# Kernel tuning notes

Measured on AMD Instinct MI355X. Metric: run time of the kernel, lower is better.

The kernel has to match this reference:

```python
import jax, jax.numpy as jnp
import numpy as np

SEQ_LEN = 4096
HIDDEN = 1280
NUM_HEADS = 16
HEAD_DIM = HIDDEN // NUM_HEADS  # 80
NUM_SEQS = 8


def setup_inputs() -> dict:
    key = jax.random.key(0)
    ks = jax.random.split(key, 8)
    x = jax.random.normal(ks[0], (SEQ_LEN, HIDDEN), dtype=jnp.float32)
    # rotary tables: use cos/sin of random angles so they are bounded like real RoPE tables
    ang = jax.random.uniform(ks[1], (SEQ_LEN, HEAD_DIM), dtype=jnp.float32) * 6.283185
    cos = jnp.cos(ang)
    sin = jnp.sin(ang)
    # variable-length packed segments: strictly increasing boundaries incl. 0 and SEQ_LEN
    rng = np.random.default_rng(0)
    inner = np.sort(rng.choice(np.arange(1, SEQ_LEN), size=NUM_SEQS - 1, replace=False))
    cu_seqlens = jnp.asarray(np.concatenate([[0], inner, [SEQ_LEN]]), dtype=jnp.int32)
    s = 0.02
    w_qkv = jax.random.normal(ks[2], (HIDDEN, 3 * HIDDEN), dtype=jnp.float32) * s
    b_qkv = jnp.zeros((3 * HIDDEN,), dtype=jnp.float32)
    w_proj = jax.random.normal(ks[3], (HIDDEN, HIDDEN), dtype=jnp.float32) * s
    b_proj = jnp.zeros((HIDDEN,), dtype=jnp.float32)
    return {"x": x, "cu_seqlens": cu_seqlens, "cos": cos, "sin": sin,
            "w_qkv": w_qkv, "b_qkv": b_qkv, "w_proj": w_proj, "b_proj": b_proj}


def _rotate_half(t):
    d = t.shape[-1] // 2
    return jnp.concatenate([-t[..., d:], t[..., :d]], axis=-1)


def _apply_rope(q, k, cos, sin):
    # q,k: (S,H,D); cos,sin: (S,D) broadcast over heads, computed in fp32
    c = cos[:, None, :].astype(jnp.float32)
    s = sin[:, None, :].astype(jnp.float32)
    qf, kf = q.astype(jnp.float32), k.astype(jnp.float32)
    q_out = qf * c + _rotate_half(qf) * s
    k_out = kf * c + _rotate_half(kf) * s
    return q_out.astype(q.dtype), k_out.astype(k.dtype)


def reference(x, cu_seqlens, cos, sin, w_qkv, b_qkv, w_proj, b_proj):
    S = x.shape[0]
    scale = HEAD_DIM ** (-0.5)
    qkv = (x @ w_qkv + b_qkv).reshape(S, 3, NUM_HEADS, HEAD_DIM)
    q, k, v = qkv[:, 0], qkv[:, 1], qkv[:, 2]  # each (S,H,D)
    q, k = _apply_rope(q, k, cos, sin)
    # block-diagonal varlen attention via segment-id mask (same math as per-chunk softmax)
    pos = jnp.arange(S)
    seg = jnp.searchsorted(cu_seqlens[1:], pos, side='right')  # (S,) segment id
    mask = seg[:, None] == seg[None, :]  # (S,S) block-diagonal
    scores = jnp.einsum('shd,thd->hst', q, k) * scale  # (H,S,S)
    scores = jnp.where(mask[None], scores.astype(jnp.float32), jnp.finfo(jnp.float32).min)
    attn = jax.nn.softmax(scores, axis=-1).astype(q.dtype)
    out = jnp.einsum('hst,thd->shd', attn, v).reshape(S, NUM_HEADS * HEAD_DIM)
    return out @ w_proj + b_proj
```

## Files before the change

kernel.cpp:

```cpp
#include <hip/hip_runtime.h>
#include <cstdint>
#include <cstddef>

typedef __bf16 bf16x8 __attribute__((ext_vector_type(8)));
typedef float f32x4 __attribute__((ext_vector_type(4)));
typedef float f32x16 __attribute__((ext_vector_type(16)));
typedef unsigned short u16x8 __attribute__((ext_vector_type(8)));

#define SEQ   4096
#define HID   1280
#define NH    16
#define HD    80

__device__ __forceinline__ unsigned short f2bf(float f) {
  unsigned int u = __float_as_uint(f);
  unsigned int r = u + 0x7FFFu + ((u >> 16) & 1u);
  return (unsigned short)(r >> 16);
}
__device__ __forceinline__ float bf2f(unsigned short h) {
  return __uint_as_float(((unsigned int)h) << 16);
}
__device__ __forceinline__ __bf16 us2bf(unsigned short u) {
  union { unsigned short s; __bf16 b; } c; c.s = u; return c.b;
}
__device__ __forceinline__ void dma16(const void* g, void* l) {
  __builtin_amdgcn_global_load_lds((const __attribute__((address_space(1))) unsigned int*)g,
                                   (__attribute__((address_space(3))) unsigned int*)l, 16, 0, 0);
}
__device__ __forceinline__ unsigned int cvtpk(float a, float b) {
  unsigned int w;
  asm("v_cvt_pk_bf16_f32 %0, %1, %2" : "=v"(w) : "v"(a), "v"(b));
  return w;
}
__device__ __forceinline__ float lo2f(unsigned int w) { return __uint_as_float(w << 16); }
__device__ __forceinline__ float hi2f(unsigned int w) { return __uint_as_float(w & 0xffff0000u); }

__global__ __launch_bounds__(256) void split_hi_kernel(const float* __restrict__ x,
                                                       unsigned short* __restrict__ hi,
                                                       int n4) {
  int i = blockIdx.x * 256 + threadIdx.x;
  if (i >= n4) return;
  float4 v = *((const float4*)x + i);
  *((ushort4*)hi + i) = make_ushort4(f2bf(v.x), f2bf(v.y), f2bf(v.z), f2bf(v.w));
}

__global__ __launch_bounds__(256) void tsplit_kernel(const float* __restrict__ W,
                                                     unsigned short* __restrict__ Thi,
                                                     unsigned short* __restrict__ Tlo,
                                                     int K, int N) {
  __shared__ float tile[32][33];
  int n0 = blockIdx.x * 32, k0 = blockIdx.y * 32;
  int tx = threadIdx.x & 31, ty = threadIdx.x >> 5;
#pragma unroll
  for (int i = 0; i < 32; i += 8)
    tile[ty + i][tx] = W[(size_t)(k0 + ty + i) * N + n0 + tx];
  __syncthreads();
#pragma unroll
  for (int i = 0; i < 32; i += 8) {
    float v = tile[tx][ty + i];
    size_t idx = (size_t)(n0 + ty + i) * K + (size_t)(k0 + tx);
    unsigned short h = f2bf(v);
    Thi[idx] = h;
    Tlo[idx] = f2bf(v - bf2f(h));
  }
}

__global__ __launch_bounds__(256, 3) void gemm128_x2(
    const unsigned short* __restrict__ A, const unsigned short* __restrict__ Bh,
    const unsigned short* __restrict__ Bl, const float* __restrict__ bias,
    float* __restrict__ out0, float* __restrict__ out1, float* __restrict__ out2,
    int M, int N, int K) {
  __shared__ __align__(16) unsigned short sALL[3 * 8192];

  const int t = threadIdx.x;
  const int lane = t & 63, wave = t >> 6;
  const int c16 = lane & 15, quad = lane >> 4;
  const int bm = blockIdx.y * 128, bn = blockIdx.x * 128;
  const int wr = (wave >> 1) * 64, wc = (wave & 1) * 64;
  const int lrow = lane >> 3;
  const int lswz = (lane & 7) ^ lrow;

  f32x4 acc[4][4];
#pragma unroll
  for (int i = 0; i < 4; ++i)
#pragma unroll
    for (int j = 0; j < 4; ++j) acc[i][j] = (f32x4){0.f, 0.f, 0.f, 0.f};

  const unsigned short* gp[12];
#pragma unroll
  for (int i = 0; i < 12; ++i) {
    const int ua = wave * 12 + i;
    const int arr = ua >> 4, sub = ua & 15;
    const unsigned short* g = (arr == 0) ? A : (arr == 1) ? Bh : Bl;
    const int rowg = ((arr == 0) ? bm : bn) + sub * 8 + lrow;
    gp[i] = g + (size_t)rowg * K + lswz * 8;
  }

  for (int k0 = 0; k0 < K; k0 += 64) {
    __syncthreads();
#pragma unroll
    for (int i = 0; i < 12; ++i)
      dma16(gp[i] + k0, &sALL[(wave * 12 + i) * 512]);
    __syncthreads();
#pragma unroll
    for (int ks = 0; ks < 2; ++ks) {
      bf16x8 a[4], bh[4], bl[4];
#pragma unroll
      for (int mi = 0; mi < 4; ++mi) {
        const int row = wr + mi * 16 + c16;
        const int off = row * 64 + (((ks * 4 + quad) ^ (row & 7)) * 8);
        a[mi] = *(const bf16x8*)&sALL[off];
      }
#pragma unroll
      for (int ni = 0; ni < 4; ++ni) {
        const int row = wc + ni * 16 + c16;
        const int off = row * 64 + (((ks * 4 + quad) ^ (row & 7)) * 8);
        bh[ni] = *(const bf16x8*)&sALL[8192 + off];
        bl[ni] = *(const bf16x8*)&sALL[16384 + off];
      }
#pragma unroll
      for (int mi = 0; mi < 4; ++mi)
#pragma unroll
        for (int ni = 0; ni < 4; ++ni) {
          acc[mi][ni] = __builtin_amdgcn_mfma_f32_16x16x32_bf16(a[mi], bh[ni], acc[mi][ni], 0, 0, 0);
          acc[mi][ni] = __builtin_amdgcn_mfma_f32_16x16x32_bf16(a[mi], bl[ni], acc[mi][ni], 0, 0, 0);
        }
    }
  }
#pragma unroll
  for (int ni = 0; ni < 4; ++ni) {
    int colg = bn + wc + ni * 16 + c16;
    float bv = bias[colg];
    float* op;
    int c = colg;
    if (c < 1280) op = out0;
    else if (c < 2560) { op = out1; c -= 1280; }
    else { op = out2; c -= 2560; }
#pragma unroll
    for (int mi = 0; mi < 4; ++mi)
#pragma unroll
      for (int r = 0; r < 4; ++r) {
        int rowg = bm + wr + mi * 16 + quad * 4 + r;
        op[(size_t)rowg * 1280 + c] = acc[mi][ni][r] + bv;
      }
  }
}

__global__ __launch_bounds__(256) void rope_pack_kernel(
    float* __restrict__ qf, const float* __restrict__ kf,
    const float* __restrict__ cs, const float* __restrict__ sn,
    unsigned short* __restrict__ khi, unsigned short* __restrict__ klo) {
  const int h = blockIdx.y;
  const int s = blockIdx.x * 64 + (threadIdx.x >> 2);
  const int p = threadIdx.x & 3;
  float* qrow = qf + (size_t)s * HID + h * HD;
  const float* krow = kf + (size_t)s * HID + h * HD;
  const float* cr = cs + (size_t)s * HD;
  const float* sr = sn + (size_t)s * HD;
  unsigned short* kh = khi + ((size_t)h * SEQ + s) * HD;
  unsigned short* kl = klo + ((size_t)h * SEQ + s) * HD;
#pragma unroll
  for (int j = 0; j < 10; ++j) {
    int d = 10 * p + j;
    float c0 = cr[d], s0 = sr[d], c1 = cr[d + 40], s1 = sr[d + 40];
    float q0 = qrow[d], q1 = qrow[d + 40];
    qrow[d]      = q0 * c0 - q1 * s0;
    qrow[d + 40] = q1 * c1 + q0 * s1;
    float k0 = krow[d], k1 = krow[d + 40];
    float kn0 = k0 * c0 - k1 * s0;
    float kn1 = k1 * c1 + k0 * s1;
    unsigned short h0 = f2bf(kn0), h1 = f2bf(kn1);
    kh[d] = h0;      kl[d] = f2bf(kn0 - bf2f(h0));
    kh[d + 40] = h1; kl[d + 40] = f2bf(kn1 - bf2f(h1));
  }
}

__global__ __launch_bounds__(256) void vt_pack_kernel(const float* __restrict__ vf,
                                                      unsigned short* __restrict__ vthi,
                                                      unsigned short* __restrict__ vtlo) {
  __shared__ unsigned short sTh[80][72];
  __shared__ unsigned short sTl[80][72];
  const int h = blockIdx.y;
  const int s0 = blockIdx.x * 64;
  const int t = threadIdx.x;
  {
    int row = t >> 2, p = (t & 3) * 20;
    const float* src = vf + (size_t)(s0 + row) * HID + h * HD + p;
#pragma unroll
    for (int i = 0; i < 5; ++i) {
      float4 v = *(const float4*)(src + 4 * i);
      float vv[4] = {v.x, v.y, v.z, v.w};
#pragma unroll
      for (int j = 0; j < 4; ++j) {
        int d = p + 4 * i + j;
        unsigned short hu = f2bf(vv[j]);
        sTh[d][row] = hu;
        sTl[d][row] = f2bf(vv[j] - bf2f(hu));
      }
    }
  }
  __syncthreads();
  if (t < 160) {
    int d = t >> 1, half = (t & 1) * 32;
    size_t base = (size_t)(h * HD + d) * SEQ + s0 + half;
#pragma unroll
    for (int i = 0; i < 8; ++i) {
      *(ushort4*)&vthi[base + 4 * i] = *(ushort4*)&sTh[d][half + 4 * i];
      *(ushort4*)&vtlo[base + 4 * i] = *(ushort4*)&sTl[d][half + 4 * i];
    }
  }
}


#define MFMA32(A, B, C) __builtin_amdgcn_mfma_f32_32x32x16_bf16(A, B, C, 0, 0, 0)

__global__ __launch_bounds__(128, 2) void attn_kernel(
    const float* __restrict__ qf, const unsigned short* __restrict__ khi,
    const unsigned short* __restrict__ klo, const unsigned short* __restrict__ vthi,
    const unsigned short* __restrict__ vtlo, const int* __restrict__ cu,
    unsigned short* __restrict__ ohi) {
  __shared__ __align__(16) unsigned short sAll[20480];
  unsigned short* const sKh = sAll;
  unsigned short* const sKl = sAll + 5120;
  unsigned short* const sVh = sAll + 10240;
  unsigned short* const sVl = sAll + 15360;

  const int t = threadIdx.x;
  const int lane = t & 63, wave = t >> 6;
  const int ln5 = lane & 31;
  const int hi  = lane >> 5;
  const int ln7 = lane & 7;
  const int lr8 = lane >> 3;
  const int vswz = (lane & 7) ^ lr8;

  const unsigned int u = (blockIdx.x & 7) * 128 + (blockIdx.x >> 3);
  const int h = (int)(u >> 6);
  const int r0 = (int)(u & 63u) * 64;

  int cu_r[9];
#pragma unroll
  for (int i = 0; i < 9; ++i) cu_r[i] = cu[i];

  const int q_my = r0 + wave * 32 + ln5;
  int sq = 0, sg0 = 0, sg1 = 0;
#pragma unroll
  for (int i = 1; i < 8; ++i) {
    sq  += (q_my    >= cu_r[i]) ? 1 : 0;
    sg0 += (r0      >= cu_r[i]) ? 1 : 0;
    sg1 += (r0 + 63 >= cu_r[i]) ? 1 : 0;
  }
  const int kb_lo = cu_r[sq], kb_hi = cu_r[sq + 1];
  const int ck0 = cu_r[sg0] & ~63;
  const int kend = cu_r[sg1 + 1];
  const int nchunk = (kend - ck0 + 63) >> 6;

  int ccol[5];
#pragma unroll
  for (int c = 0; c < 5; ++c)
    ccol[c] = (c < 4) ? ((((2 * c) + hi) ^ ln7) * 8) : ((8 + hi) * 8);

  int koff[10];
#pragma unroll
  for (int i = 0; i < 10; ++i) {
    const int G = i * 64 + lane;
    const int key = (G * 205) >> 11;
    const int p = G - key * 10;
    const int cl = (p < 8) ? (p ^ (key & 7)) : p;
    koff[i] = key * 80 + cl * 8;
  }

  const float qsc = 0.11180339887498949f;
  bf16x8 qh[5], ql[5];
  {
    const float* qrow = qf + (size_t)q_my * HID + h * HD;
#pragma unroll
    for (int kt = 0; kt < 5; ++kt) {
      const int d0 = kt * 16 + hi * 8;
      float4 a0 = *(const float4*)(qrow + d0);
      float4 a1 = *(const float4*)(qrow + d0 + 4);
      float va[8] = {a0.x, a0.y, a0.z, a0.w, a1.x, a1.y, a1.z, a1.w};
      bf16x8 hf, lf;
#pragma unroll
      for (int j = 0; j < 8; ++j) {
        float v = va[j] * qsc;
        unsigned short hu = f2bf(v);
        hf[j] = us2bf(hu);
        lf[j] = us2bf(f2bf(v - bf2f(hu)));
      }
      qh[kt] = hf; ql[kt] = lf;
    }
  }

  f32x16 O0, O1, O2;
#pragma unroll
  for (int r = 0; r < 16; ++r) { O0[r] = 0.f; O1[r] = 0.f; O2[r] = 0.f; }
  float m_i = -1e30f, l_i = 0.f;

  auto STAGE_K = [&](int ck) {
    const unsigned short* gk = (wave & 1) ? klo : khi;
    unsigned short* lk = (wave & 1) ? sKl : sKh;
    const unsigned short* gb = gk + ((size_t)h * SEQ + ck) * 80;
#pragma unroll
    for (int i2 = 0; i2 < 10; ++i2) dma16(gb + koff[i2], lk + i2 * 512);
  };
  auto STAGE_V = [&](int ck) {
    const unsigned short* gv = (wave & 1) ? vtlo : vthi;
    unsigned short* lv = (wave & 1) ? sVl : sVh;
#pragma unroll
    for (int i2 = 0; i2 < 10; ++i2)
      dma16(gv + (size_t)(h * HD + 8 * i2 + lr8) * SEQ + ck + vswz * 8, lv + i2 * 512);
  };

  STAGE_K(ck0);
  STAGE_V(ck0);
  __syncthreads();

  for (int ci = 0; ci < nchunk; ++ci) {
    const int ck = ck0 + ci * 64;

    f32x16 sc0, sc1;
#pragma unroll
    for (int r = 0; r < 16; ++r) { sc0[r] = 0.f; sc1[r] = 0.f; }
    __builtin_amdgcn_s_setprio(1);
#pragma unroll
    for (int kd = 0; kd < 5; ++kd) {
      const int col = ccol[kd];
      bf16x8 kha = *(const bf16x8*)&sKh[ln5 * 80 + col];
      bf16x8 kla = *(const bf16x8*)&sKl[ln5 * 80 + col];
      bf16x8 khb = *(const bf16x8*)&sKh[(32 + ln5) * 80 + col];
      bf16x8 klb = *(const bf16x8*)&sKl[(32 + ln5) * 80 + col];
      sc0 = MFMA32(kha, qh[kd], sc0); sc1 = MFMA32(khb, qh[kd], sc1);
      sc0 = MFMA32(kha, ql[kd], sc0); sc1 = MFMA32(khb, ql[kd], sc1);
      sc0 = MFMA32(kla, qh[kd], sc0); sc1 = MFMA32(klb, qh[kd], sc1);
    }
    __builtin_amdgcn_s_setprio(0);

    float mx = -1e30f;
#define MSK(SCV, KT2)                                                          \
    {                                                                          \
      const int kb = ck + (KT2) * 32 + 4 * hi;                                 \
      _Pragma("unroll")                                                        \
      for (int r = 0; r < 16; ++r) {                                           \
        const int kg = kb + (r & 3) + 8 * (r >> 2);                            \
        float v = (kg >= kb_lo && kg < kb_hi) ? SCV[r] : -1e30f;               \
        SCV[r] = v;                                                            \
        mx = fmaxf(mx, v);                                                     \
      }                                                                        \
    }
    MSK(sc0, 0)
    MSK(sc1, 1)
#undef MSK
    mx = fmaxf(mx, __shfl_xor(mx, 32));
    const float mnew = fmaxf(m_i, mx);
    const float alpha = __expf(m_i - mnew);
    float ps = 0.f;
#define EXPP(SCV)                                                              \
    _Pragma("unroll")                                                          \
    for (int r = 0; r < 16; ++r) {                                             \
      const float s = SCV[r];                                                  \
      const float p = (s > -1e29f) ? __expf(s - mnew) : 0.f;                   \
      ps += p;                                                                 \
      SCV[r] = p;                                                              \
    }
    EXPP(sc0)
    EXPP(sc1)
#undef EXPP
    ps += __shfl_xor(ps, 32);
    l_i = l_i * alpha + ps;
    m_i = mnew;
#pragma unroll
    for (int r = 0; r < 16; ++r) { O0[r] *= alpha; O1[r] *= alpha; O2[r] *= alpha; }

    __syncthreads();
    if (ci + 1 < nchunk) STAGE_K(ck + 64);

    __builtin_amdgcn_s_setprio(1);
#define PV_STEP(SCV, SUB, KT)                                                  \
    {                                                                          \
      unsigned int A1 = cvtpk(SCV[(SUB)*8+0], SCV[(SUB)*8+1]);                 \
      unsigned int A2 = cvtpk(SCV[(SUB)*8+2], SCV[(SUB)*8+3]);                 \
      unsigned int B1 = cvtpk(SCV[(SUB)*8+4], SCV[(SUB)*8+5]);                 \
      unsigned int B2 = cvtpk(SCV[(SUB)*8+6], SCV[(SUB)*8+7]);                 \
      float e0 = SCV[(SUB)*8+0] - lo2f(A1), e1 = SCV[(SUB)*8+1] - hi2f(A1);    \
      float e2 = SCV[(SUB)*8+2] - lo2f(A2), e3 = SCV[(SUB)*8+3] - hi2f(A2);    \
      float e4 = SCV[(SUB)*8+4] - lo2f(B1), e5 = SCV[(SUB)*8+5] - hi2f(B1);    \
      float e6 = SCV[(SUB)*8+6] - lo2f(B2), e7 = SCV[(SUB)*8+7] - hi2f(B2);    \
      unsigned int C1 = cvtpk(e0, e1), C2 = cvtpk(e2, e3);                     \
      unsigned int D1 = cvtpk(e4, e5), D2 = cvtpk(e6, e7);                     \
      unsigned int T1 = (unsigned int)__shfl_xor((int)(hi ? A1 : B1), 32);     \
      unsigned int T2 = (unsigned int)__shfl_xor((int)(hi ? A2 : B2), 32);     \
      unsigned int U1 = (unsigned int)__shfl_xor((int)(hi ? C1 : D1), 32);     \
      unsigned int U2 = (unsigned int)__shfl_xor((int)(hi ? C2 : D2), 32);     \
      union { unsigned int w[4]; bf16x8 v; } ph_, pl_;                         \
      ph_.w[0] = hi ? T1 : A1;  ph_.w[1] = hi ? T2 : A2;                       \
      ph_.w[2] = hi ? B1 : T1;  ph_.w[3] = hi ? B2 : T2;                       \
      pl_.w[0] = hi ? U1 : C1;  pl_.w[1] = hi ? U2 : C2;                       \
      pl_.w[2] = hi ? D1 : U1;  pl_.w[3] = hi ? D2 : U2;                       \
      const int vc = ccol[KT];                                                 \
      bf16x8 vh0 = *(const bf16x8*)&sVh[ln5 * 64 + vc];                        \
      bf16x8 vh1 = *(const bf16x8*)&sVh[(32 + ln5) * 64 + vc];                 \
      bf16x8 vh2 = *(const bf16x8*)&sVh[(64 + (ln5 & 15)) * 64 + vc];          \
      bf16x8 vl0 = *(const bf16x8*)&sVl[ln5 * 64 + vc];                        \
      bf16x8 vl1 = *(const bf16x8*)&sVl[(32 + ln5) * 64 + vc];                 \
      bf16x8 vl2 = *(const bf16x8*)&sVl[(64 + (ln5 & 15)) * 64 + vc];          \
      O0 = MFMA32(vh0, ph_.v, O0); O1 = MFMA32(vh1, ph_.v, O1);                \
      O2 = MFMA32(vh2, ph_.v, O2);                                             \
      O0 = MFMA32(vl0, ph_.v, O0); O1 = MFMA32(vl1, ph_.v, O1);                \
      O2 = MFMA32(vl2, ph_.v, O2);                                             \
      O0 = MFMA32(vh0, pl_.v, O0); O1 = MFMA32(vh1, pl_.v, O1);                \
      O2 = MFMA32(vh2, pl_.v, O2);                                             \
    }
    PV_STEP(sc0, 0, 0)
    PV_STEP(sc0, 1, 1)
    PV_STEP(sc1, 0, 2)
    PV_STEP(sc1, 1, 3)
#undef PV_STEP
    __builtin_amdgcn_s_setprio(0);

    __syncthreads();
    if (ci + 1 < nchunk) STAGE_V(ck + 64);
  }

  const float inv = 1.0f / l_i;
  unsigned short* tr = sAll + wave * 3072;
#define WR(OV, DT)                                                             \
  _Pragma("unroll")                                                            \
  for (int r = 0; r < 16; r += 2) {                                            \
    if ((DT) < 2 || r < 8) {                                                   \
      const int d = (DT) * 32 + (r & 3) + 8 * (r >> 2) + 4 * hi;               \
      unsigned int w = cvtpk(OV[r] * inv, OV[r + 1] * inv);                    \
      *(unsigned int*)&tr[ln5 * 96 + d] = w;                                   \
    }                                                                          \
  }
  WR(O0, 0)
  WR(O1, 1)
  WR(O2, 2)
#undef WR
  __syncthreads();
  {
    const int qq = lane >> 1, part = lane & 1;
    const unsigned short* src = tr + qq * 96 + part * 40;
    unsigned short* dst = ohi + (size_t)(r0 + wave * 32 + qq) * HID + h * HD + part * 40;
#pragma unroll
    for (int i = 0; i < 5; ++i)
      *(u16x8*)&dst[i * 8] = *(const u16x8*)&src[i * 8];
  }
}

extern "C" void kernel_launch(void* const* d_in, const int* in_sizes, int n_in,
                              void* d_out, int out_size, void* d_ws, size_t ws_size,
                              hipStream_t stream) {
  const float* x      = (const float*)d_in[0];
  const int*   cu     = (const int*)d_in[1];
  const float* cs     = (const float*)d_in[2];
  const float* sn     = (const float*)d_in[3];
  const float* w_qkv  = (const float*)d_in[4];
  const float* b_qkv  = (const float*)d_in[5];
  const float* w_proj = (const float*)d_in[6];
  const float* b_proj = (const float*)d_in[7];
  float* out = (float*)d_out;

  char* ws = (char*)d_ws;
  float*          qf     = (float*)(ws + 0);
  float*          kf     = (float*)(ws + 20971520ULL);
  unsigned short* vthi   = (unsigned short*)(ws + 20971520ULL);
  unsigned short* vtlo   = (unsigned short*)(ws + 31457280ULL);
  float*          vf     = (float*)(ws + 41943040ULL);
  unsigned short* o_hi   = (unsigned short*)(ws + 41943040ULL);
  unsigned short* x_hi   = (unsigned short*)(ws + 62914560ULL);
  unsigned short* khi    = (unsigned short*)(ws + 62914560ULL);
  unsigned short* klo    = (unsigned short*)(ws + 73400320ULL);
  unsigned short* wqt_hi = (unsigned short*)(ws + 83886080ULL);
  unsigned short* wqt_lo = (unsigned short*)(ws + 93716480ULL);
  unsigned short* wpt_hi = (unsigned short*)(ws + 103546880ULL);
  unsigned short* wpt_lo = (unsigned short*)(ws + 106823680ULL);

  split_hi_kernel<<<5120, 256, 0, stream>>>(x, x_hi, 1310720);
  tsplit_kernel<<<dim3(120, 40), 256, 0, stream>>>(w_qkv, wqt_hi, wqt_lo, 1280, 3840);
  tsplit_kernel<<<dim3(40, 40), 256, 0, stream>>>(w_proj, wpt_hi, wpt_lo, 1280, 1280);
  gemm128_x2<<<dim3(30, 32), 256, 0, stream>>>(x_hi, wqt_hi, wqt_lo, b_qkv,
                                               qf, kf, vf, 4096, 3840, 1280);
  rope_pack_kernel<<<dim3(64, 16), 256, 0, stream>>>(qf, kf, cs, sn, khi, klo);
  vt_pack_kernel<<<dim3(64, 16), 256, 0, stream>>>(vf, vthi, vtlo);
  attn_kernel<<<1024, 128, 0, stream>>>(qf, khi, klo, vthi, vtlo, cu, o_hi);
  gemm128_x2<<<dim3(10, 32), 256, 0, stream>>>(o_hi, wpt_hi, wpt_lo, b_proj,
                                               out, nullptr, nullptr, 4096, 1280, 1280);
}
```

Before: 369.0 us.

## Make attention persistent with per-XCD atomic work queue sorted by cost

Adds a small scheduling kernel that computes per-tile chunk counts from cu_seqlens and builds a longest-first permutation for each XCD. The attention kernel becomes persistent (768 blocks) and pulls tiles from per-XCD atomic counters, which is meant to fix load imbalance across variable-length segments. It also folds log2(e) into the Q scale so exp2f replaces __expf, and writes output directly from registers instead of staging it through LDS. The costs are an extra launch, atomics and barriers per tile, and scattered 8-byte global stores.

```diff
diff --git a/kernel.cpp b/kernel.cpp
--- a/kernel.cpp
+++ b/kernel.cpp
@@ -5,7 +5,6 @@
 typedef __bf16 bf16x8 __attribute__((ext_vector_type(8)));
 typedef float f32x4 __attribute__((ext_vector_type(4)));
 typedef float f32x16 __attribute__((ext_vector_type(16)));
-typedef unsigned short u16x8 __attribute__((ext_vector_type(8)));
 
 #define SEQ   4096
 #define HID   1280
@@ -211,6 +210,41 @@
   }
 }
 
+__global__ __launch_bounds__(128) void sched_kernel(const int* __restrict__ cu,
+                                                    int* __restrict__ perm,
+                                                    unsigned int* __restrict__ ctr) {
+  __shared__ int w[64];
+  const int t = threadIdx.x;
+  if (t < 8) ctr[t * 16] = 0u;
+  int cu_r[9];
+#pragma unroll
+  for (int i = 0; i < 9; ++i) cu_r[i] = cu[i];
+  if (t < 64) {
+    const int r0 = t * 64;
+    int sg0 = 0, sg1 = 0;
+#pragma unroll
+    for (int i = 1; i < 8; ++i) {
+      sg0 += (r0      >= cu_r[i]) ? 1 : 0;
+      sg1 += (r0 + 63 >= cu_r[i]) ? 1 : 0;
+    }
+    const int ck0 = cu_r[sg0] & ~63;
+    const int kend = cu_r[sg1 + 1];
+    w[t] = (kend - ck0 + 63) >> 6;
+  }
+  __syncthreads();
+  if (t < 64) {
+    const int wt = w[t];
+    int rank = 0;
+    for (int i = 0; i < 64; ++i)
+      rank += ((w[i] > wt) || (w[i] == wt && i < t)) ? 1 : 0;
+#pragma unroll
+    for (int x = 0; x < 8; ++x) {
+      perm[x * 128 + rank * 2 + 0] = (2 * x) * 64 + t;
+      perm[x * 128 + rank * 2 + 1] = (2 * x + 1) * 64 + t;
+    }
+  }
+}
+
 
 #define MFMA32(A, B, C) __builtin_amdgcn_mfma_f32_32x32x16_bf16(A, B, C, 0, 0, 0)
 
@@ -218,46 +252,25 @@
     const float* __restrict__ qf, const unsigned short* __restrict__ khi,
     const unsigned short* __restrict__ klo, const unsigned short* __restrict__ vthi,
     const unsigned short* __restrict__ vtlo, const int* __restrict__ cu,
-    unsigned short* __restrict__ ohi) {
+    unsigned short* __restrict__ ohi, const int* __restrict__ perm,
+    unsigned int* __restrict__ ctr) {
   __shared__ __align__(16) unsigned short sAll[20480];
   unsigned short* const sKh = sAll;
   unsigned short* const sKl = sAll + 5120;
   unsigned short* const sVh = sAll + 10240;
   unsigned short* const sVl = sAll + 15360;
+  unsigned int* const s_u = (unsigned int*)sAll;
 
   const int t = threadIdx.x;
   const int lane = t & 63, wave = t >> 6;
   const int ln5 = lane & 31;
   const int hi  = lane >> 5;
   const int ln7 = lane & 7;
-  const int lr8 = lane >> 3;
-  const int vswz = (lane & 7) ^ lr8;
-
-  const unsigned int u = (blockIdx.x & 7) * 128 + (blockIdx.x >> 3);
-  const int h = (int)(u >> 6);
-  const int r0 = (int)(u & 63u) * 64;
+  const int xcd = blockIdx.x & 7;
 
   int cu_r[9];
 #pragma unroll
   for (int i = 0; i < 9; ++i) cu_r[i] = cu[i];
-
-  const int q_my = r0 + wave * 32 + ln5;
-  int sq = 0, sg0 = 0, sg1 = 0;
-#pragma unroll
-  for (int i = 1; i < 8; ++i) {
-    sq  += (q_my    >= cu_r[i]) ? 1 : 0;
-    sg0 += (r0      >= cu_r[i]) ? 1 : 0;
-    sg1 += (r0 + 63 >= cu_r[i]) ? 1 : 0;
-  }
-  const int kb_lo = cu_r[sq], kb_hi = cu_r[sq + 1];
-  const int ck0 = cu_r[sg0] & ~63;
-  const int kend = cu_r[sg1 + 1];
-  const int nchunk = (kend - ck0 + 63) >> 6;
-
-  int ccol[5];
-#pragma unroll
-  for (int c = 0; c < 5; ++c)
-    ccol[c] = (c < 4) ? ((((2 * c) + hi) ^ ln7) * 8) : ((8 + hi) * 8);
 
   int koff[10];
 #pragma unroll
@@ -268,182 +281,225 @@
     const int cl = (p < 8) ? (p ^ (key & 7)) : p;
     koff[i] = key * 80 + cl * 8;
   }
-
-  const float qsc = 0.11180339887498949f;
-  bf16x8 qh[5], ql[5];
-  {
-    const float* qrow = qf + (size_t)q_my * HID + h * HD;
-#pragma unroll
-    for (int kt = 0; kt < 5; ++kt) {
-      const int d0 = kt * 16 + hi * 8;
-      float4 a0 = *(const float4*)(qrow + d0);
-      float4 a1 = *(const float4*)(qrow + d0 + 4);
-      float va[8] = {a0.x, a0.y, a0.z, a0.w, a1.x, a1.y, a1.z, a1.w};
-      bf16x8 hf, lf;
-#pragma unroll
-      for (int j = 0; j < 8; ++j) {
-        float v = va[j] * qsc;
-        unsigned short hu = f2bf(v);
-        hf[j] = us2bf(hu);
-        lf[j] = us2bf(f2bf(v - bf2f(hu)));
-      }
-      qh[kt] = hf; ql[kt] = lf;
-    }
-  }
-
-  f32x16 O0, O1, O2;
-#pragma unroll
-  for (int r = 0; r < 16; ++r) { O0[r] = 0.f; O1[r] = 0.f; O2[r] = 0.f; }
-  float m_i = -1e30f, l_i = 0.f;
-
-  auto STAGE_K = [&](int ck) {
-    const unsigned short* gk = (wave & 1) ? klo : khi;
-    unsigned short* lk = (wave & 1) ? sKl : sKh;
-    const unsigned short* gb = gk + ((size_t)h * SEQ + ck) * 80;
-#pragma unroll
-    for (int i2 = 0; i2 < 10; ++i2) dma16(gb + koff[i2], lk + i2 * 512);
-  };
-  auto STAGE_V = [&](int ck) {
-    const unsigned short* gv = (wave & 1) ? vtlo : vthi;
-    unsigned short* lv = (wave & 1) ? sVl : sVh;
-#pragma unroll
-    for (int i2 = 0; i2 < 10; ++i2)
-      dma16(gv + (size_t)(h * HD + 8 * i2 + lr8) * SEQ + ck + vswz * 8, lv + i2 * 512);
-  };
-
-  STAGE_K(ck0);
-  STAGE_V(ck0);
-  __syncthreads();
-
-  for (int ci = 0; ci < nchunk; ++ci) {
-    const int ck = ck0 + ci * 64;
-
-    f32x16 sc0, sc1;
-#pragma unroll
-    for (int r = 0; r < 16; ++r) { sc0[r] = 0.f; sc1[r] = 0.f; }
-    __builtin_amdgcn_s_setprio(1);
-#pragma unroll
-    for (int kd = 0; kd < 5; ++kd) {
-      const int col = ccol[kd];
-      bf16x8 kha = *(const bf16x8*)&sKh[ln5 * 80 + col];
-      bf16x8 kla = *(const bf16x8*)&sKl[ln5 * 80 + col];
-      bf16x8 khb = *(const bf16x8*)&sKh[(32 + ln5) * 80 + col];
-      bf16x8 klb = *(const bf16x8*)&sKl[(32 + ln5) * 80 + col];
-      sc0 = MFMA32(kha, qh[kd], sc0); sc1 = MFMA32(khb, qh[kd], sc1);
-      sc0 = MFMA32(kha, ql[kd], sc0); sc1 = MFMA32(khb, ql[kd], sc1);
-      sc0 = MFMA32(kla, qh[kd], sc0); sc1 = MFMA32(klb, qh[kd], sc1);
-    }
-    __builtin_amdgcn_s_setprio(0);
-
-    float mx = -1e30f;
+  int voff[10];
+#pragma unroll
+  for (int i = 0; i < 10; ++i) {
+    const int G = i * 64 + lane;
+    const int d = G >> 3, gc = G & 7;
+    const int g = gc ^ (d & 7);
+    voff[i] = d * SEQ + g * 8;
+  }
+  int ccol[5];
+#pragma unroll
+  for (int c = 0; c < 5; ++c)
+    ccol[c] = (c < 4) ? ((((2 * c) + hi) ^ ln7) * 8) : ((8 + hi) * 8);
+  int gcol[4];
+#pragma unroll
+  for (int c = 0; c < 4; ++c)
+    gcol[c] = (((2 * c) + hi) ^ ln7) * 8;
+
+  const float qsc = 0.11180339887498949f * 1.4426950408889634f;
+
+  for (;;) {
+    __syncthreads();
+    if (t == 0) s_u[0] = atomicAdd(&ctr[xcd * 16], 1u);
+    __syncthreads();
+    const unsigned int idx = s_u[0];
+    if (idx >= 128u) break;
+    const int uu = perm[xcd * 128 + idx];
+    const int h = uu >> 6;
+    const int r0 = (uu & 63) * 64;
+
+    const int q_my = r0 + wave * 32 + ln5;
+    int sq = 0, sg0 = 0, sg1 = 0;
+#pragma unroll
+    for (int i = 1; i < 8; ++i) {
+      sq  += (q_my    >= cu_r[i]) ? 1 : 0;
+      sg0 += (r0      >= cu_r[i]) ? 1 : 0;
+      sg1 += (r0 + 63 >= cu_r[i]) ? 1 : 0;
+    }
+    const int kb_lo = cu_r[sq], kb_hi = cu_r[sq + 1];
+    const int ck0 = cu_r[sg0] & ~63;
+    const int kend = cu_r[sg1 + 1];
+    const int nchunk = (kend - ck0 + 63) >> 6;
+
+    bf16x8 qh[5], ql[5];
+    {
+      const float* qrow = qf + (size_t)q_my * HID + h * HD;
+#pragma unroll
+      for (int kt = 0; kt < 5; ++kt) {
+        const int d0 = kt * 16 + hi * 8;
+        float4 a0 = *(const float4*)(qrow + d0);
+        float4 a1 = *(const float4*)(qrow + d0 + 4);
+        float va[8] = {a0.x, a0.y, a0.z, a0.w, a1.x, a1.y, a1.z, a1.w};
+        bf16x8 hf, lf;
+#pragma unroll
+        for (int j = 0; j < 8; ++j) {
+          float v = va[j] * qsc;
+          unsigned short hu = f2bf(v);
+          hf[j] = us2bf(hu);
+          lf[j] = us2bf(f2bf(v - bf2f(hu)));
+        }
+        qh[kt] = hf; ql[kt] = lf;
+      }
+    }
+
+    f32x16 O0, O1, O2;
+#pragma unroll
+    for (int r = 0; r < 16; ++r) { O0[r] = 0.f; O1[r] = 0.f; O2[r] = 0.f; }
+    float m_i = -1e30f, l_i = 0.f;
+
+    const unsigned short* gkh = khi + (size_t)h * SEQ * 80;
+    const unsigned short* gkl = klo + (size_t)h * SEQ * 80;
+    const unsigned short* gvh = vthi + (size_t)h * HD * SEQ;
+    const unsigned short* gvl = vtlo + (size_t)h * HD * SEQ;
+
+    auto STAGE_K = [&](int ck) {
+      const unsigned short* gb = (wave ? gkl : gkh) + (size_t)ck * 80;
+      unsigned short* lk = wave ? sKl : sKh;
+#pragma unroll
+      for (int i = 0; i < 10; ++i) dma16(gb + koff[i], lk + i * 512);
+    };
+    auto STAGE_V = [&](int ck) {
+      const unsigned short* gb = wave ? gvl : gvh;
+      unsigned short* lv = wave ? sVl : sVh;
+#pragma unroll
+      for (int i = 0; i < 10; ++i) dma16(gb + ck + voff[i], lv + i * 512);
+    };
+
+    STAGE_K(ck0);
+    STAGE_V(ck0);
+    __syncthreads();
+
+    for (int ci = 0; ci < nchunk; ++ci) {
+      const int ck = ck0 + ci * 64;
+
+      f32x16 sc0, sc1;
+#pragma unroll
+      for (int r = 0; r < 16; ++r) { sc0[r] = 0.f; sc1[r] = 0.f; }
+      __builtin_amdgcn_s_setprio(1);
+#pragma unroll
+      for (int kd = 0; kd < 5; ++kd) {
+        const int col = ccol[kd];
+        bf16x8 kha = *(const bf16x8*)&sKh[ln5 * 80 + col];
+        bf16x8 kla = *(const bf16x8*)&sKl[ln5 * 80 + col];
+        bf16x8 khb = *(const bf16x8*)&sKh[(32 + ln5) * 80 + col];
+        bf16x8 klb = *(const bf16x8*)&sKl[(32 + ln5) * 80 + col];
+        sc0 = MFMA32(kha, qh[kd], sc0); sc1 = MFMA32(khb, qh[kd], sc1);
+        sc0 = MFMA32(kha, ql[kd], sc0); sc1 = MFMA32(khb, ql[kd], sc1);
+        sc0 = MFMA32(kla, qh[kd], sc0); sc1 = MFMA32(klb, qh[kd], sc1);
+      }
+      __builtin_amdgcn_s_setprio(0);
+
+      float mx = -1e30f;
 #define MSK(SCV, KT2)                                                          \
-    {                                                                          \
-      const int kb = ck + (KT2) * 32 + 4 * hi;                                 \
+      {                                                                        \
+        const int kb = ck + (KT2) * 32 + 4 * hi;                               \
+        _Pragma("unroll")                                                      \
+        for (int r = 0; r < 16; ++r) {                                         \
+          const int kg = kb + (r & 3) + 8 * (r >> 2);                          \
+          float v = (kg >= kb_lo && kg < kb_hi) ? SCV[r] : -1e30f;             \
+          SCV[r] = v;                                                          \
+          mx = fmaxf(mx, v);                                                   \
+        }                                                                      \
+      }
+      MSK(sc0, 0)
+      MSK(sc1, 1)
+#undef MSK
+      mx = fmaxf(mx, __shfl_xor(mx, 32));
+      const float mnew = fmaxf(m_i, mx);
+      const float alpha = exp2f(m_i - mnew);
+      float ps = 0.f;
+#define EXPP(SCV)                                                              \
       _Pragma("unroll")                                                        \
       for (int r = 0; r < 16; ++r) {                                           \
-        const int kg = kb + (r & 3) + 8 * (r >> 2);                            \
-        float v = (kg >= kb_lo && kg < kb_hi) ? SCV[r] : -1e30f;               \
-        SCV[r] = v;                                                            \
-        mx = fmaxf(mx, v);                                                     \
-      }                                                                        \
-    }
-    MSK(sc0, 0)
-    MSK(sc1, 1)
-#undef MSK
-    mx = fmaxf(mx, __shfl_xor(mx, 32));
-    const float mnew = fmaxf(m_i, mx);
-    const float alpha = __expf(m_i - mnew);
-    float ps = 0.f;
-#define EXPP(SCV)                                                              \
-    _Pragma("unroll")                                                          \
-    for (int r = 0; r < 16; ++r) {                                             \
-      const float s = SCV[r];                                                  \
-      const float p = (s > -1e29f) ? __expf(s - mnew) : 0.f;                   \
-      ps += p;                                                                 \
-      SCV[r] = p;                                                              \
-    }
-    EXPP(sc0)
-    EXPP(sc1)
+        const float s = SCV[r];                                                \
+        const float p = (s > -1e29f) ? exp2f(s - mnew) : 0.f;                  \
+        ps += p;                                                               \
+        SCV[r] = p;                                                            \
+      }
+      EXPP(sc0)
+      EXPP(sc1)
 #undef EXPP
-    ps += __shfl_xor(ps, 32);
-    l_i = l_i * alpha + ps;
-    m_i = mnew;
-#pragma unroll
-    for (int r = 0; r < 16; ++r) { O0[r] *= alpha; O1[r] *= alpha; O2[r] *= alpha; }
-
-    __syncthreads();
-    if (ci + 1 < nchunk) STAGE_K(ck + 64);
-
-    __builtin_amdgcn_s_setprio(1);
-#define PV_STEP(SCV, SUB, KT)                                                  \
-    {                                                                          \
-      unsigned int A1 = cvtpk(SCV[(SUB)*8+0], SCV[(SUB)*8+1]);                 \
-      unsigned int A2 = cvtpk(SCV[(SUB)*8+2], SCV[(SUB)*8+3]);                 \
-      unsigned int B1 = cvtpk(SCV[(SUB)*8+4], SCV[(SUB)*8+5]);                 \
-      unsigned int B2 = cvtpk(SCV[(SUB)*8+6], SCV[(SUB)*8+7]);                 \
-      float e0 = SCV[(SUB)*8+0] - lo2f(A1), e1 = SCV[(SUB)*8+1] - hi2f(A1);    \
-      float e2 = SCV[(SUB)*8+2] - lo2f(A2), e3 = SCV[(SUB)*8+3] - hi2f(A2);    \
-      float e4 = SCV[(SUB)*8+4] - lo2f(B1), e5 = SCV[(SUB)*8+5] - hi2f(B1);    \
-      float e6 = SCV[(SUB)*8+6] - lo2f(B2), e7 = SCV[(SUB)*8+7] - hi2f(B2);    \
-      unsigned int C1 = cvtpk(e0, e1), C2 = cvtpk(e2, e3);                     \
-      unsigned int D1 = cvtpk(e4, e5), D2 = cvtpk(e6, e7);                     \
-      unsigned int T1 = (unsigned int)__shfl_xor((int)(hi ? A1 : B1), 32);     \
-      unsigned int T2 = (unsigned int)__shfl_xor((int)(hi ? A2 : B2), 32);     \
-      unsigned int U1 = (unsigned int)__shfl_xor((int)(hi ? C1 : D1), 32);     \
-      unsigned int U2 = (unsigned int)__shfl_xor((int)(hi ? C2 : D2), 32);     \
-      union { unsigned int w[4]; bf16x8 v; } ph_, pl_;                         \
-      ph_.w[0] = hi ? T1 : A1;  ph_.w[1] = hi ? T2 : A2;                       \
-      ph_.w[2] = hi ? B1 : T1;  ph_.w[3] = hi ? B2 : T2;                       \
-      pl_.w[0] = hi ? U1 : C1;  pl_.w[1] = hi ? U2 : C2;                       \
-      pl_.w[2] = hi ? D1 : U1;  pl_.w[3] = hi ? D2 : U2;                       \
-      const int vc = ccol[KT];                                                 \
-      bf16x8 vh0 = *(const bf16x8*)&sVh[ln5 * 64 + vc];                        \
-      bf16x8 vh1 = *(const bf16x8*)&sVh[(32 + ln5) * 64 + vc];                 \
-      bf16x8 vh2 = *(const bf16x8*)&sVh[(64 + (ln5 & 15)) * 64 + vc];          \
-      bf16x8 vl0 = *(const bf16x8*)&sVl[ln5 * 64 + vc];                        \
-      bf16x8 vl1 = *(const bf16x8*)&sVl[(32 + ln5) * 64 + vc];                 \
-      bf16x8 vl2 = *(const bf16x8*)&sVl[(64 + (ln5 & 15)) * 64 + vc];          \
-      O0 = MFMA32(vh0, ph_.v, O0); O1 = MFMA32(vh1, ph_.v, O1);                \
-      O2 = MFMA32(vh2, ph_.v, O2);                                             \
-      O0 = MFMA32(vl0, ph_.v, O0); O1 = MFMA32(vl1, ph_.v, O1);                \
-      O2 = MFMA32(vl2, ph_.v, O2);                                             \
-      O0 = MFMA32(vh0, pl_.v, O0); O1 = MFMA32(vh1, pl_.v, O1);                \
-      O2 = MFMA32(vh2, pl_.v, O2);                                             \
-    }
-    PV_STEP(sc0, 0, 0)
-    PV_STEP(sc0, 1, 1)
-    PV_STEP(sc1, 0, 2)
-    PV_STEP(sc1, 1, 3)
+      ps += __shfl_xor(ps, 32);
+      l_i = l_i * alpha + ps;
+      m_i = mnew;
+#pragma unroll
+      for (int r = 0; r < 16; ++r) { O0[r] *= alpha; O1[r] *= alpha; O2[r] *= alpha; }
+
+      __syncthreads();
+      if (ci + 1 < nchunk) STAGE_K(ck + 64);
+
+      __builtin_amdgcn_s_setprio(1);
+#define PV_STEP(SCV, SUB, J)                                                   \
+      {                                                                        \
+        unsigned int A1 = cvtpk(SCV[(SUB)*8+0], SCV[(SUB)*8+1]);               \
+        unsigned int A2 = cvtpk(SCV[(SUB)*8+2], SCV[(SUB)*8+3]);               \
+        unsigned int B1 = cvtpk(SCV[(SUB)*8+4], SCV[(SUB)*8+5]);               \
+        unsigned int B2 = cvtpk(SCV[(SUB)*8+6], SCV[(SUB)*8+7]);               \
+        float e0 = SCV[(SUB)*8+0] - lo2f(A1), e1 = SCV[(SUB)*8+1] - hi2f(A1);  \
+        float e2 = SCV[(SUB)*8+2] - lo2f(A2), e3 = SCV[(SUB)*8+3] - hi2f(A2);  \
+        float e4 = SCV[(SUB)*8+4] - lo2f(B1), e5 = SCV[(SUB)*8+5] - hi2f(B1);  \
+        float e6 = SCV[(SUB)*8+6] - lo2f(B2), e7 = SCV[(SUB)*8+7] - hi2f(B2);  \
+        unsigned int C1 = cvtpk(e0, e1), C2 = cvtpk(e2, e3);                   \
+        unsigned int D1 = cvtpk(e4, e5), D2 = cvtpk(e6, e7);                   \
+        unsigned int T1 = (unsigned int)__shfl_xor((int)(hi ? A1 : B1), 32);   \
+        unsigned int T2 = (unsigned int)__shfl_xor((int)(hi ? A2 : B2), 32);   \
+        unsigned int U1 = (unsigned int)__shfl_xor((int)(hi ? C1 : D1), 32);   \
+        unsigned int U2 = (unsigned int)__shfl_xor((int)(hi ? C2 : D2), 32);   \
+        union { unsigned int w[4]; bf16x8 v; } ph_, pl_;                       \
+        ph_.w[0] = hi ? T1 : A1;  ph_.w[1] = hi ? T2 : A2;                     \
+        ph_.w[2] = hi ? B1 : T1;  ph_.w[3] = hi ? B2 : T2;                     \
+        pl_.w[0] = hi ? U1 : C1;  pl_.w[1] = hi ? U2 : C2;                     \
+        pl_.w[2] = hi ? D1 : U1;  pl_.w[3] = hi ? D2 : U2;                     \
+        const int vc = gcol[J];                                                \
+        bf16x8 vh0 = *(const bf16x8*)&sVh[ln5 * 64 + vc];                      \
+        bf16x8 vh1 = *(const bf16x8*)&sVh[(32 + ln5) * 64 + vc];               \
+        bf16x8 vh2 = *(const bf16x8*)&sVh[(64 + (ln5 & 15)) * 64 + vc];        \
+        bf16x8 vl0 = *(const bf16x8*)&sVl[ln5 * 64 + vc];                      \
+        bf16x8 vl1 = *(const bf16x8*)&sVl[(32 + ln5) * 64 + vc];               \
+        bf16x8 vl2 = *(const bf16x8*)&sVl[(64 + (ln5 & 15)) * 64 + vc];        \
+        O0 = MFMA32(vh0, ph_.v, O0); O1 = MFMA32(vh1, ph_.v, O1);              \
+        O2 = MFMA32(vh2, ph_.v, O2);                                           \
+        O0 = MFMA32(vl0, ph_.v, O0); O1 = MFMA32(vl1, ph_.v, O1);              \
+        O2 = MFMA32(vl2, ph_.v, O2);                                           \
+        O0 = MFMA32(vh0, pl_.v, O0); O1 = MFMA32(vh1, pl_.v, O1);              \
+        O2 = MFMA32(vh2, pl_.v, O2);                                           \
+      }
+      PV_STEP(sc0, 0, 0)
+      PV_STEP(sc0, 1, 1)
+      PV_STEP(sc1, 0, 2)
+      PV_STEP(sc1, 1, 3)
 #undef PV_STEP
-    __builtin_amdgcn_s_setprio(0);
-
-    __syncthreads();
-    if (ci + 1 < nchunk) STAGE_V(ck + 64);
-  }
-
-  const float inv = 1.0f / l_i;
-  unsigned short* tr = sAll + wave * 3072;
-#define WR(OV, DT)                                                             \
-  _Pragma("unroll")                                                            \
-  for (int r = 0; r < 16; r += 2) {                                            \
-    if ((DT) < 2 || r < 8) {                                                   \
-      const int d = (DT) * 32 + (r & 3) + 8 * (r >> 2) + 4 * hi;               \
-      unsigned int w = cvtpk(OV[r] * inv, OV[r + 1] * inv);                    \
-      *(unsigned int*)&tr[ln5 * 96 + d] = w;                                   \
-    }                                                                          \
-  }
-  WR(O0, 0)
-  WR(O1, 1)
-  WR(O2, 2)
-#undef WR
-  __syncthreads();
-  {
-    const int qq = lane >> 1, part = lane & 1;
-    const unsigned short* src = tr + qq * 96 + part * 40;
-    unsigned short* dst = ohi + (size_t)(r0 + wave * 32 + qq) * HID + h * HD + part * 40;
-#pragma unroll
-    for (int i = 0; i < 5; ++i)
-      *(u16x8*)&dst[i * 8] = *(const u16x8*)&src[i * 8];
+      __builtin_amdgcn_s_setprio(0);
+
+      __syncthreads();
+      if (ci + 1 < nchunk) STAGE_V(ck + 64);
+    }
+
+    const float inv = 1.0f / l_i;
+    unsigned short* orow = ohi + (size_t)q_my * HID + h * HD + 4 * hi;
+#pragma unroll
+    for (int j = 0; j < 4; ++j) {
+      unsigned long long w =
+          (unsigned long long)cvtpk(O0[4 * j] * inv, O0[4 * j + 1] * inv) |
+          ((unsigned long long)cvtpk(O0[4 * j + 2] * inv, O0[4 * j + 3] * inv) << 32);
+      *(unsigned long long*)&orow[8 * j] = w;
+    }
+#pragma unroll
+    for (int j = 0; j < 4; ++j) {
+      unsigned long long w =
+          (unsigned long long)cvtpk(O1[4 * j] * inv, O1[4 * j + 1] * inv) |
+          ((unsigned long long)cvtpk(O1[4 * j + 2] * inv, O1[4 * j + 3] * inv) << 32);
+      *(unsigned long long*)&orow[32 + 8 * j] = w;
+    }
+#pragma unroll
+    for (int j = 0; j < 2; ++j) {
+      unsigned long long w =
+          (unsigned long long)cvtpk(O2[4 * j] * inv, O2[4 * j + 1] * inv) |
+          ((unsigned long long)cvtpk(O2[4 * j + 2] * inv, O2[4 * j + 3] * inv) << 32);
+      *(unsigned long long*)&orow[64 + 8 * j] = w;
+    }
   }
 }
 
@@ -474,6 +530,8 @@
   unsigned short* wqt_lo = (unsigned short*)(ws + 93716480ULL);
   unsigned short* wpt_hi = (unsigned short*)(ws + 103546880ULL);
   unsigned short* wpt_lo = (unsigned short*)(ws + 106823680ULL);
+  unsigned int*   ctr    = (unsigned int*)(ws + 83886080ULL);
+  int*            perm   = (int*)(ws + 83886080ULL + 1024);
 
   split_hi_kernel<<<5120, 256, 0, stream>>>(x, x_hi, 1310720);
   tsplit_kernel<<<dim3(120, 40), 256, 0, stream>>>(w_qkv, wqt_hi, wqt_lo, 1280, 3840);
@@ -482,7 +540,8 @@
                                                qf, kf, vf, 4096, 3840, 1280);
   rope_pack_kernel<<<dim3(64, 16), 256, 0, stream>>>(qf, kf, cs, sn, khi, klo);
   vt_pack_kernel<<<dim3(64, 16), 256, 0, stream>>>(vf, vthi, vtlo);
-  attn_kernel<<<1024, 128, 0, stream>>>(qf, khi, klo, vthi, vtlo, cu, o_hi);
+  sched_kernel<<<1, 128, 0, stream>>>(cu, perm, ctr);
+  attn_kernel<<<768, 128, 0, stream>>>(qf, khi, klo, vthi, vtlo, cu, o_hi, perm, ctr);
   gemm128_x2<<<dim3(10, 32), 256, 0, stream>>>(o_hi, wpt_hi, wpt_lo, b_proj,
                                                out, nullptr, nullptr, 4096, 1280, 1280);
 }
```

Result: no change. 370.6 us (+0.4%).

## Schedule attention tiles by descending work with snake assignment across XCDs

Applied to the files above, without the earlier changes.

Adds a tiny scheduling kernel that computes each 64-row query tile's key-chunk count from cu_seqlens, ranks the tiles by that work, and builds a permutation. It assigns heaviest tiles first in a snake pattern, interleaved across the 8 XCD slots. The attention kernel reads its (head, row-tile) from this permutation instead of a fixed mapping. The aim is to balance variable-length segment work across CUs and reduce tail imbalance. The cost is an extra single-block launch and one indirect load per block, and the perm buffer reuses the wqt_hi workspace region after the QKV GEMM has finished with it.

```diff
diff --git a/kernel.cpp b/kernel.cpp
--- a/kernel.cpp
+++ b/kernel.cpp
@@ -211,6 +211,46 @@
   }
 }
 
+__global__ __launch_bounds__(64) void sched_kernel(const int* __restrict__ cu,
+                                                   int* __restrict__ perm) {
+  __shared__ int w[64];
+  __shared__ int tile_of_rank[64];
+  const int t = threadIdx.x;
+  int cu_r[9];
+#pragma unroll
+  for (int i = 0; i < 9; ++i) cu_r[i] = cu[i];
+  {
+    const int r0 = t * 64;
+    int sg0 = 0, sg1 = 0;
+#pragma unroll
+    for (int i = 1; i < 8; ++i) {
+      sg0 += (r0      >= cu_r[i]) ? 1 : 0;
+      sg1 += (r0 + 63 >= cu_r[i]) ? 1 : 0;
+    }
+    const int ck0 = cu_r[sg0] & ~63;
+    const int kend = cu_r[sg1 + 1];
+    w[t] = (kend - ck0 + 63) >> 6;
+  }
+  __syncthreads();
+  {
+    const int wt = w[t];
+    int rank = 0;
+    for (int i = 0; i < 64; ++i)
+      rank += ((w[i] > wt) || (w[i] == wt && i < t)) ? 1 : 0;
+    tile_of_rank[rank] = t;
+  }
+  __syncthreads();
+  for (int s = t; s < 128; s += 64) {
+    const int j = s & 31, g = s >> 5;
+    const int f = (g == 0) ? j : (g == 1) ? (63 - j) : (g == 2) ? (64 + j) : (127 - j);
+    const int tau = tile_of_rank[f >> 1];
+    const int p = f & 1;
+#pragma unroll
+    for (int x = 0; x < 8; ++x)
+      perm[x * 128 + s] = (2 * x + p) * 64 + tau;
+  }
+}
+
 
 #define MFMA32(A, B, C) __builtin_amdgcn_mfma_f32_32x32x16_bf16(A, B, C, 0, 0, 0)
 
@@ -218,7 +258,7 @@
     const float* __restrict__ qf, const unsigned short* __restrict__ khi,
     const unsigned short* __restrict__ klo, const unsigned short* __restrict__ vthi,
     const unsigned short* __restrict__ vtlo, const int* __restrict__ cu,
-    unsigned short* __restrict__ ohi) {
+    unsigned short* __restrict__ ohi, const int* __restrict__ perm) {
   __shared__ __align__(16) unsigned short sAll[20480];
   unsigned short* const sKh = sAll;
   unsigned short* const sKl = sAll + 5120;
@@ -233,9 +273,9 @@
   const int lr8 = lane >> 3;
   const int vswz = (lane & 7) ^ lr8;
 
-  const unsigned int u = (blockIdx.x & 7) * 128 + (blockIdx.x >> 3);
-  const int h = (int)(u >> 6);
-  const int r0 = (int)(u & 63u) * 64;
+  const int u = perm[(blockIdx.x & 7) * 128 + (blockIdx.x >> 3)];
+  const int h = u >> 6;
+  const int r0 = (u & 63) * 64;
 
   int cu_r[9];
 #pragma unroll
@@ -474,6 +514,7 @@
   unsigned short* wqt_lo = (unsigned short*)(ws + 93716480ULL);
   unsigned short* wpt_hi = (unsigned short*)(ws + 103546880ULL);
   unsigned short* wpt_lo = (unsigned short*)(ws + 106823680ULL);
+  int*            perm   = (int*)(ws + 83886080ULL);
 
   split_hi_kernel<<<5120, 256, 0, stream>>>(x, x_hi, 1310720);
   tsplit_kernel<<<dim3(120, 40), 256, 0, stream>>>(w_qkv, wqt_hi, wqt_lo, 1280, 3840);
@@ -482,7 +523,8 @@
                                                qf, kf, vf, 4096, 3840, 1280);
   rope_pack_kernel<<<dim3(64, 16), 256, 0, stream>>>(qf, kf, cs, sn, khi, klo);
   vt_pack_kernel<<<dim3(64, 16), 256, 0, stream>>>(vf, vthi, vtlo);
-  attn_kernel<<<1024, 128, 0, stream>>>(qf, khi, klo, vthi, vtlo, cu, o_hi);
+  sched_kernel<<<1, 64, 0, stream>>>(cu, perm);
+  attn_kernel<<<1024, 128, 0, stream>>>(qf, khi, klo, vthi, vtlo, cu, o_hi, perm);
   gemm128_x2<<<dim3(10, 32), 256, 0, stream>>>(o_hi, wpt_hi, wpt_lo, b_proj,
                                                out, nullptr, nullptr, 4096, 1280, 1280);
 }
```

Result: no change. 368.9 us (-0.0%).
